# Performance work log

Measured on AMD Instinct MI355X. Metric: run time of the kernel, lower is better.

Reference implementation:

```python
import jax, jax.numpy as jnp
import numpy as np

N, M, D = 8192, 8192, 64

def setup_inputs() -> dict:
    key = jax.random.key(0)
    kx, ky = jax.random.split(key)
    x = jax.random.normal(kx, (N, D), dtype=jnp.float32)
    y = jax.random.normal(ky, (M, D), dtype=jnp.float32)
    return {"x": x, "y": y}

def reference(x, y):
    T = 1.0
    # Dmat = 2 - euclidean cdist(x, y), computed via the Gram trick.
    sq = (jnp.sum(x * x, axis=1)[:, None]
          + jnp.sum(y * y, axis=1)[None, :]
          - 2.0 * (x @ y.T))
    Dmat = 2.0 - jnp.sqrt(jnp.maximum(sq, 0.0))          # [N, M]
    logprob_rows = jax.nn.log_softmax(Dmat * T, axis=1)   # [N, M]
    logprob_cols = jax.nn.log_softmax(Dmat.T * T, axis=1) # [M, N]
    choice_rows = jnp.argmax(logprob_rows, axis=1)        # [N]
    choice_cols = jnp.argmax(logprob_cols, axis=1)        # [M]
    seq = jnp.arange(M, dtype=choice_cols.dtype)
    mutual = choice_rows[choice_cols] == seq              # [M] bool
    lp_rows = jnp.take_along_axis(logprob_rows, choice_rows[:, None], axis=1)[:, 0]  # [N]
    lp_cols = jnp.take_along_axis(logprob_cols, choice_cols[:, None], axis=1)[:, 0]  # [M]
    # Padded (jit-friendly) form of the boolean compaction: entries where
    # mutual is False are zeroed; mutual mask identifies valid matches.
    log_probs = jnp.where(mutual, lp_rows[choice_cols] + lp_cols, 0.0)  # [M]
    dmatches = jnp.stack([choice_cols, seq], axis=1)      # [M, 2]
    return (log_probs, dmatches, mutual)
```

## Files before the change

### kernel.cpp

```cpp
#include <hip/hip_runtime.h>
#include <stdint.h>

#define NROWS 8192
#define MCOLS 8192
#define DDIM  64
#define NBX   32
#define NBY   64

typedef _Float16 half8   __attribute__((ext_vector_type(8)));
typedef float    floatx4 __attribute__((ext_vector_type(4)));

__device__ __forceinline__ unsigned f2key(float f) {
  unsigned u = __float_as_uint(f);
  return (u & 0x80000000u) ? ~u : (u | 0x80000000u);
}
__device__ __forceinline__ float key2f(unsigned k) {
  unsigned u = (k & 0x80000000u) ? (k & 0x7fffffffu) : ~k;
  return __uint_as_float(u);
}

__global__ void convert_kernel(const float* __restrict__ x, const float* __restrict__ y,
                               _Float16* __restrict__ xh, _Float16* __restrict__ xl,
                               _Float16* __restrict__ yh, _Float16* __restrict__ yl,
                               float* __restrict__ xn, float* __restrict__ yn) {
  __shared__ float lnorm[32];
  const int gid = blockIdx.x * 256 + threadIdx.x;
  if (threadIdx.x < 32) lnorm[threadIdx.x] = 0.0f;
  __syncthreads();

  const float* src; _Float16 *dh, *dl; float* nout; int t, rowbase;
  if (gid < 65536) { src = x; dh = xh; dl = xl; nout = xn; t = gid;
                     rowbase = blockIdx.x * 32; }
  else             { src = y; dh = yh; dl = yl; nout = yn; t = gid - 65536;
                     rowbase = (blockIdx.x - 256) * 32; }

  const int lane = t & 63;
  const int c    = (t >> 6) & 1;
  const int p    = t >> 7;
  const int row  = p * 16 + (lane & 15);
  const int k0   = c * 32 + ((lane >> 4) << 3);
  const float* s = src + (size_t)row * DDIM + k0;

  float fb[8];
  *(floatx4*)(&fb[0]) = *(const floatx4*)(s);
  *(floatx4*)(&fb[4]) = *(const floatx4*)(s + 4);

  _Float16 hbuf[8], lbuf[8];
  float s8 = 0.0f;
  #pragma unroll
  for (int j = 0; j < 8; ++j) {
    float f = fb[j];
    _Float16 h = (_Float16)f;
    hbuf[j] = h;
    lbuf[j] = (_Float16)((f - (float)h) * 2048.0f);
    s8 = fmaf(f, f, s8);
  }
  size_t o = (size_t)t * 8;
  *(half8*)(dh + o) = *(half8*)hbuf;
  *(half8*)(dl + o) = *(half8*)lbuf;

  atomicAdd(&lnorm[((p & 1) << 4) | (t & 15)], s8);
  __syncthreads();
  if (threadIdx.x < 32) nout[rowbase + threadIdx.x] = lnorm[threadIdx.x];
}

#define MFMA16(A, B, C) __builtin_amdgcn_mfma_f32_16x16x32_f16((A), (B), (C), 0, 0, 0)

__global__ __launch_bounds__(256, 3) void mfma_tile_kernel(
    const _Float16* __restrict__ xh, const _Float16* __restrict__ xl,
    const _Float16* __restrict__ yh, const _Float16* __restrict__ yl,
    const float* __restrict__ xn, const float* __restrict__ yn,
    unsigned long long* __restrict__ row_part_key, float* __restrict__ row_part_sum,
    unsigned long long* __restrict__ col_part_key, float* __restrict__ col_part_sum)
{
  __shared__ unsigned long long lkey[256];
  __shared__ float              lsum[256];

  const int wave = threadIdx.x >> 6;
  const int lane = threadIdx.x & 63;
  const int l15  = lane & 15;
  const int g    = lane >> 4;
  const int ap0  = blockIdx.y * 8 + wave * 2;
  const int ro   = ap0 * 16 + g * 4;
  const int colbase = blockIdx.x * 256;

  lkey[threadIdx.x] = 0ull;
  lsum[threadIdx.x] = 0.0f;
  __syncthreads();

  const half8* xh8 = (const half8*)xh;
  const half8* xl8 = (const half8*)xl;
  const half8* yh8 = (const half8*)yh;
  const half8* yl8 = (const half8*)yl;
  const size_t a0 = (size_t)ap0 * 128 + lane;
  half8 Ah[2][2], Al[2][2];
  #pragma unroll
  for (int p = 0; p < 2; ++p) {
    Ah[p][0] = xh8[a0 + p * 128];      Ah[p][1] = xh8[a0 + p * 128 + 64];
    Al[p][0] = xl8[a0 + p * 128];      Al[p][1] = xl8[a0 + p * 128 + 64];
  }

  float xne[8], rsum[8], rmax[8]; int ridx[8];
  #pragma unroll
  for (int s = 0; s < 8; ++s) {
    xne[s]  = xn[ro + ((s >> 2) << 4) + (s & 3)];
    rsum[s] = 0.0f; rmax[s] = -3.4e38f; ridx[s] = 0;
  }

  const size_t bcol0 = (size_t)(blockIdx.x * 16) * 128 + lane;

  half8 b0h0, b0h1, b0l0, b0l1; float y0n;
  half8 b1h0, b1h1, b1l0, b1l1; float y1n;
  b0h0 = yh8[bcol0];        b0h1 = yh8[bcol0 + 64];
  b0l0 = yl8[bcol0];        b0l1 = yl8[bcol0 + 64];
  y0n  = yn[colbase + l15];
  b1h0 = yh8[bcol0 + 128];  b1h1 = yh8[bcol0 + 192];
  b1l0 = yl8[bcol0 + 128];  b1l1 = yl8[bcol0 + 192];
  y1n  = yn[colbase + 16 + l15];

#define MFMA_TILE(BH0, BH1, BL0, BL1, O1A, O2A, O1B, O2B)                      \
  {                                                                            \
    floatx4 c1_ = {}, c2_ = {};                                                \
    c1_ = MFMA16(Ah[0][0], BH0, c1_);                                          \
    c1_ = MFMA16(Ah[0][1], BH1, c1_);                                          \
    c2_ = MFMA16(Al[0][0], BH0, c2_);                                          \
    c2_ = MFMA16(Al[0][1], BH1, c2_);                                          \
    c2_ = MFMA16(Ah[0][0], BL0, c2_);                                          \
    c2_ = MFMA16(Ah[0][1], BL1, c2_);                                          \
    O1A = c1_; O2A = c2_;                                                      \
    floatx4 d1_ = {}, d2_ = {};                                                \
    d1_ = MFMA16(Ah[1][0], BH0, d1_);                                          \
    d1_ = MFMA16(Ah[1][1], BH1, d1_);                                          \
    d2_ = MFMA16(Al[1][0], BH0, d2_);                                          \
    d2_ = MFMA16(Al[1][1], BH1, d2_);                                          \
    d2_ = MFMA16(Ah[1][0], BL0, d2_);                                          \
    d2_ = MFMA16(Ah[1][1], BL1, d2_);                                          \
    O1B = d1_; O2B = d2_;                                                      \
  }

#define EPILOGUE(JT, C1A, C2A, C1B, C2B, YNC)                                  \
  {                                                                            \
    const int col_ = colbase + (JT) * 16 + l15;                                \
    float cmax_ = -3.4e38f; int cidx_ = 0;                                     \
    float epan0_, epan1_;                                                      \
    {                                                                          \
      float ee_[4];                                                            \
      _Pragma("unroll")                                                        \
      for (int r = 0; r < 4; ++r) {                                            \
        const int s_ = r;                                                      \
        float dot = fmaf(C2A[r], (1.0f / 2048.0f), C1A[r]);                    \
        float sq  = fmaxf(fmaf(-2.0f, dot, xne[s_] + (YNC)), 0.0f);            \
        float d   = 2.0f - __builtin_amdgcn_sqrtf(sq);                         \
        float e   = __expf(d);                                                 \
        rsum[s_] += e;                                                         \
        if (d > rmax[s_]) ridx[s_] = col_;       \
        rmax[s_] = fmaxf(rmax[s_], d);                                         \
        if (d > cmax_) cidx_ = s_;               \
        cmax_ = fmaxf(cmax_, d);                                               \
        ee_[r] = e;                                                            \
      }                                                                        \
      epan0_ = (ee_[0] + ee_[1]) + (ee_[2] + ee_[3]);                          \
    }                                                                          \
    {                                                                          \
      float ee_[4];                                                            \
      _Pragma("unroll")                                                        \
      for (int r = 0; r < 4; ++r) {                                            \
        const int s_ = 4 + r;                                                  \
        float dot = fmaf(C2B[r], (1.0f / 2048.0f), C1B[r]);                    \
        float sq  = fmaxf(fmaf(-2.0f, dot, xne[s_] + (YNC)), 0.0f);            \
        float d   = 2.0f - __builtin_amdgcn_sqrtf(sq);                         \
        float e   = __expf(d);                                                 \
        rsum[s_] += e;                                                         \
        if (d > rmax[s_]) ridx[s_] = col_;                                     \
        rmax[s_] = fmaxf(rmax[s_], d);                                         \
        if (d > cmax_) cidx_ = s_;                                             \
        cmax_ = fmaxf(cmax_, d);                                               \
        ee_[r] = e;                                                            \
      }                                                                        \
      epan1_ = (ee_[0] + ee_[1]) + (ee_[2] + ee_[3]);                          \
    }                                                                          \
    float csum_ = epan0_ + epan1_;                \
    int crow_ = ro + ((cidx_ >> 2) << 4) + (cidx_ & 3);                        \
    unsigned long long ckey_ =                                                 \
        ((unsigned long long)f2key(cmax_) << 32) |                             \
        (unsigned long long)(unsigned)(~(unsigned)crow_);                      \
    atomicMax(&lkey[(JT) * 16 + l15], ckey_);                  \
    atomicAdd(&lsum[(JT) * 16 + l15], csum_);                  \
  }

  floatx4 Pc1a, Pc2a, Pc1b, Pc2b;
  floatx4 Qc1a, Qc2a, Qc1b, Qc2b;

  MFMA_TILE(b0h0, b0h1, b0l0, b0l1, Pc1a, Pc2a, Pc1b, Pc2b);

  for (int jt = 0; jt < 14; jt += 2) {
    {
      float ycur = y0n;
      const size_t bn = bcol0 + (size_t)(jt + 2) * 128;
      b0h0 = yh8[bn];      b0h1 = yh8[bn + 64];
      b0l0 = yl8[bn];      b0l1 = yl8[bn + 64];
      y0n  = yn[colbase + (jt + 2) * 16 + l15];
      MFMA_TILE(b1h0, b1h1, b1l0, b1l1, Qc1a, Qc2a, Qc1b, Qc2b);
      EPILOGUE(jt, Pc1a, Pc2a, Pc1b, Pc2b, ycur);
    }
    {
      float ycur = y1n;
      const size_t bn = bcol0 + (size_t)(jt + 3) * 128;
      b1h0 = yh8[bn];      b1h1 = yh8[bn + 64];
      b1l0 = yl8[bn];      b1l1 = yl8[bn + 64];
      y1n  = yn[colbase + (jt + 3) * 16 + l15];
      MFMA_TILE(b0h0, b0h1, b0l0, b0l1, Pc1a, Pc2a, Pc1b, Pc2b);
      EPILOGUE(jt + 1, Qc1a, Qc2a, Qc1b, Qc2b, ycur);
    }
  }
  {
    MFMA_TILE(b1h0, b1h1, b1l0, b1l1, Qc1a, Qc2a, Qc1b, Qc2b);
    EPILOGUE(14, Pc1a, Pc2a, Pc1b, Pc2b, y0n);
  }
  EPILOGUE(15, Qc1a, Qc2a, Qc1b, Qc2b, y1n);

#undef MFMA_TILE
#undef EPILOGUE

  unsigned long long rkk[8];
  #pragma unroll
  for (int s = 0; s < 8; ++s)
    rkk[s] = ((unsigned long long)f2key(rmax[s]) << 32) |
             (unsigned long long)(unsigned)(~(unsigned)ridx[s]);
  #pragma unroll
  for (int off = 1; off < 16; off <<= 1) {
    #pragma unroll
    for (int s = 0; s < 8; ++s) {
      rsum[s] += __shfl_xor(rsum[s], off);
      unsigned long long o = __shfl_xor(rkk[s], off);
      if (o > rkk[s]) rkk[s] = o;
    }
  }
  if (l15 == 0) {
    #pragma unroll
    for (int s = 0; s < 8; ++s) {
      int row = ro + ((s >> 2) << 4) + (s & 3);
      row_part_key[(size_t)blockIdx.x * NROWS + row] = rkk[s];
      row_part_sum[(size_t)blockIdx.x * NROWS + row] = rsum[s];
    }
  }

  __syncthreads();
  {
    int col = colbase + threadIdx.x;
    col_part_key[(size_t)blockIdx.y * MCOLS + col] = lkey[threadIdx.x];
    col_part_sum[(size_t)blockIdx.y * MCOLS + col] = lsum[threadIdx.x];
  }
}

__global__ __launch_bounds__(256) void reduce_rows_kernel(
    const unsigned long long* __restrict__ rpk,
    const float* __restrict__ rps,
    unsigned long long* __restrict__ row_key,
    float* __restrict__ row_sum)
{
  const int t   = blockIdx.x * 256 + threadIdx.x;
  const int row = t >> 3;
  const int i   = t & 7;
  unsigned long long best = 0ull; float sum = 0.0f;
  #pragma unroll
  for (int k = 0; k < 4; ++k) {
    const int bx = i + k * 8;
    unsigned long long kk = rpk[(size_t)bx * NROWS + row];
    if (kk > best) best = kk;
    sum += rps[(size_t)bx * NROWS + row];
  }
  #pragma unroll
  for (int off = 1; off < 8; off <<= 1) {
    sum += __shfl_xor(sum, off);
    unsigned long long o = __shfl_xor(best, off);
    if (o > best) best = o;
  }
  if (i == 0) { row_key[row] = best; row_sum[row] = sum; }
}

__global__ __launch_bounds__(256) void finalize_kernel(
    const unsigned long long* __restrict__ row_key,
    const float* __restrict__ row_sum,
    const unsigned long long* __restrict__ cpk,
    const float* __restrict__ cps,
    float* __restrict__ out)
{
  const int t = blockIdx.x * 256 + threadIdx.x;
  const int j = t >> 3;
  const int i = t & 7;

  unsigned long long ck = 0ull; float csum = 0.0f;
  #pragma unroll
  for (int k = 0; k < 8; ++k) {
    const int by = i + k * 8;
    unsigned long long kk = cpk[(size_t)by * MCOLS + j];
    if (kk > ck) ck = kk;
    csum += cps[(size_t)by * MCOLS + j];
  }
  #pragma unroll
  for (int off = 1; off < 8; off <<= 1) {
    csum += __shfl_xor(csum, off);
    unsigned long long o = __shfl_xor(ck, off);
    if (o > ck) ck = o;
  }
  if (i != 0) return;

  int   ci   = (int)(~(unsigned)ck);
  float cmax = key2f((unsigned)(ck >> 32));
  float lp_col = cmax - logf(csum);

  unsigned long long rk = row_key[ci];
  int   rj   = (int)(~(unsigned)rk);
  float rmax = key2f((unsigned)(rk >> 32));
  float lp_row = rmax - logf(row_sum[ci]);

  int mut = (rj == j);
  out[j]                 = mut ? (lp_row + lp_col) : 0.0f;
  out[MCOLS + 2 * j + 0] = (float)ci;
  out[MCOLS + 2 * j + 1] = (float)j;
  out[3 * MCOLS + j]     = mut ? 1.0f : 0.0f;
}

extern "C" void kernel_launch(void* const* d_in, const int* in_sizes, int n_in,
                              void* d_out, int out_size, void* d_ws, size_t ws_size,
                              hipStream_t stream) {
  const float* x = (const float*)d_in[0];
  const float* y = (const float*)d_in[1];
  float* out = (float*)d_out;

  char* ws = (char*)d_ws;
  unsigned long long* row_key = (unsigned long long*)(ws);
  float* row_sum = (float*)(ws + 65536);
  float* xn      = (float*)(ws + 98304);
  float* yn      = (float*)(ws + 131072);
  unsigned long long* rpk = (unsigned long long*)(ws + 163840);
  float* rps     = (float*)(ws + 2260992);
  unsigned long long* cpk = (unsigned long long*)(ws + 3309568);
  float* cps     = (float*)(ws + 7503872);
  _Float16* xh = (_Float16*)(ws + 9601024);
  _Float16* xl = (_Float16*)(ws + 10649600);
  _Float16* yh = (_Float16*)(ws + 11698176);
  _Float16* yl = (_Float16*)(ws + 12746752);

  convert_kernel<<<512, 256, 0, stream>>>(x, y, xh, xl, yh, yl, xn, yn);
  dim3 grid(MCOLS / 256, NROWS / 128);
  mfma_tile_kernel<<<grid, 256, 0, stream>>>(xh, xl, yh, yl, xn, yn,
                                             rpk, rps, cpk, cps);
  reduce_rows_kernel<<<256, 256, 0, stream>>>(rpk, rps, row_key, row_sum);
  finalize_kernel<<<256, 256, 0, stream>>>(row_key, row_sum, cpk, cps, out);
}
```

Measured before the change: 123.5 us.

## Split row panels across eight waves and fuse row reduction into finalize

The main tile kernel now launches 512 threads per block, with each wave handling a single 16-row panel instead of two. This lowers per-wave register pressure and raises latency hiding, at the cost of loading the B fragments twice as often per block. The separate row-reduction kernel is removed. Finalize instead reduces the partial row keys and sums only for each column's chosen row, which saves a launch and a full pass over the row partials.

```diff
diff --git a/kernel.cpp b/kernel.cpp
--- a/kernel.cpp
+++ b/kernel.cpp
@@ -66,7 +66,7 @@
 
 #define MFMA16(A, B, C) __builtin_amdgcn_mfma_f32_16x16x32_f16((A), (B), (C), 0, 0, 0)
 
-__global__ __launch_bounds__(256, 3) void mfma_tile_kernel(
+__global__ __launch_bounds__(512, 2) void mfma_tile_kernel(
     const _Float16* __restrict__ xh, const _Float16* __restrict__ xl,
     const _Float16* __restrict__ yh, const _Float16* __restrict__ yl,
     const float* __restrict__ xn, const float* __restrict__ yn,
@@ -80,30 +80,25 @@
   const int lane = threadIdx.x & 63;
   const int l15  = lane & 15;
   const int g    = lane >> 4;
-  const int ap0  = blockIdx.y * 8 + wave * 2;
-  const int ro   = ap0 * 16 + g * 4;
+  const int ap   = blockIdx.y * 8 + wave;
+  const int ro   = ap * 16 + g * 4;
   const int colbase = blockIdx.x * 256;
 
-  lkey[threadIdx.x] = 0ull;
-  lsum[threadIdx.x] = 0.0f;
+  if (threadIdx.x < 256) { lkey[threadIdx.x] = 0ull; lsum[threadIdx.x] = 0.0f; }
   __syncthreads();
 
   const half8* xh8 = (const half8*)xh;
   const half8* xl8 = (const half8*)xl;
   const half8* yh8 = (const half8*)yh;
   const half8* yl8 = (const half8*)yl;
-  const size_t a0 = (size_t)ap0 * 128 + lane;
-  half8 Ah[2][2], Al[2][2];
-  #pragma unroll
-  for (int p = 0; p < 2; ++p) {
-    Ah[p][0] = xh8[a0 + p * 128];      Ah[p][1] = xh8[a0 + p * 128 + 64];
-    Al[p][0] = xl8[a0 + p * 128];      Al[p][1] = xl8[a0 + p * 128 + 64];
-  }
-
-  float xne[8], rsum[8], rmax[8]; int ridx[8];
-  #pragma unroll
-  for (int s = 0; s < 8; ++s) {
-    xne[s]  = xn[ro + ((s >> 2) << 4) + (s & 3)];
+  const size_t a0 = (size_t)ap * 128 + lane;
+  half8 Ah0 = xh8[a0], Ah1 = xh8[a0 + 64];
+  half8 Al0 = xl8[a0], Al1 = xl8[a0 + 64];
+
+  float xne[4], rsum[4], rmax[4]; int ridx[4];
+  #pragma unroll
+  for (int s = 0; s < 4; ++s) {
+    xne[s]  = xn[ro + s];
     rsum[s] = 0.0f; rmax[s] = -3.4e38f; ridx[s] = 0;
   }
 
@@ -118,69 +113,38 @@
   b1l0 = yl8[bcol0 + 128];  b1l1 = yl8[bcol0 + 192];
   y1n  = yn[colbase + 16 + l15];
 
-#define MFMA_TILE(BH0, BH1, BL0, BL1, O1A, O2A, O1B, O2B)                      \
+#define MFMA_TILE(BH0, BH1, BL0, BL1, O1, O2)                                  \
   {                                                                            \
     floatx4 c1_ = {}, c2_ = {};                                                \
-    c1_ = MFMA16(Ah[0][0], BH0, c1_);                                          \
-    c1_ = MFMA16(Ah[0][1], BH1, c1_);                                          \
-    c2_ = MFMA16(Al[0][0], BH0, c2_);                                          \
-    c2_ = MFMA16(Al[0][1], BH1, c2_);                                          \
-    c2_ = MFMA16(Ah[0][0], BL0, c2_);                                          \
-    c2_ = MFMA16(Ah[0][1], BL1, c2_);                                          \
-    O1A = c1_; O2A = c2_;                                                      \
-    floatx4 d1_ = {}, d2_ = {};                                                \
-    d1_ = MFMA16(Ah[1][0], BH0, d1_);                                          \
-    d1_ = MFMA16(Ah[1][1], BH1, d1_);                                          \
-    d2_ = MFMA16(Al[1][0], BH0, d2_);                                          \
-    d2_ = MFMA16(Al[1][1], BH1, d2_);                                          \
-    d2_ = MFMA16(Ah[1][0], BL0, d2_);                                          \
-    d2_ = MFMA16(Ah[1][1], BL1, d2_);                                          \
-    O1B = d1_; O2B = d2_;                                                      \
-  }
-
-#define EPILOGUE(JT, C1A, C2A, C1B, C2B, YNC)                                  \
+    c1_ = MFMA16(Ah0, BH0, c1_);                                               \
+    c1_ = MFMA16(Ah1, BH1, c1_);                                               \
+    c2_ = MFMA16(Al0, BH0, c2_);                                               \
+    c2_ = MFMA16(Al1, BH1, c2_);                                               \
+    c2_ = MFMA16(Ah0, BL0, c2_);                                               \
+    c2_ = MFMA16(Ah1, BL1, c2_);                                               \
+    O1 = c1_; O2 = c2_;                                                        \
+  }
+
+#define EPILOGUE(JT, C1, C2, YNC)                                              \
   {                                                                            \
     const int col_ = colbase + (JT) * 16 + l15;                                \
     float cmax_ = -3.4e38f; int cidx_ = 0;                                     \
-    float epan0_, epan1_;                                                      \
-    {                                                                          \
-      float ee_[4];                                                            \
-      _Pragma("unroll")                                                        \
-      for (int r = 0; r < 4; ++r) {                                            \
-        const int s_ = r;                                                      \
-        float dot = fmaf(C2A[r], (1.0f / 2048.0f), C1A[r]);                    \
-        float sq  = fmaxf(fmaf(-2.0f, dot, xne[s_] + (YNC)), 0.0f);            \
-        float d   = 2.0f - __builtin_amdgcn_sqrtf(sq);                         \
-        float e   = __expf(d);                                                 \
-        rsum[s_] += e;                                                         \
-        if (d > rmax[s_]) ridx[s_] = col_;       \
-        rmax[s_] = fmaxf(rmax[s_], d);                                         \
-        if (d > cmax_) cidx_ = s_;               \
-        cmax_ = fmaxf(cmax_, d);                                               \
-        ee_[r] = e;                                                            \
-      }                                                                        \
-      epan0_ = (ee_[0] + ee_[1]) + (ee_[2] + ee_[3]);                          \
+    float ee_[4];                                                              \
+    _Pragma("unroll")                                                          \
+    for (int r = 0; r < 4; ++r) {                                              \
+      float dot = fmaf(C2[r], (1.0f / 2048.0f), C1[r]);                        \
+      float sq  = fmaxf(fmaf(-2.0f, dot, xne[r] + (YNC)), 0.0f);               \
+      float d   = 2.0f - __builtin_amdgcn_sqrtf(sq);                           \
+      float e   = __expf(d);                                                   \
+      rsum[r] += e;                                                            \
+      if (d > rmax[r]) ridx[r] = col_;           \
+      rmax[r] = fmaxf(rmax[r], d);                                             \
+      if (d > cmax_) cidx_ = r;                  \
+      cmax_ = fmaxf(cmax_, d);                                                 \
+      ee_[r] = e;                                                              \
     }                                                                          \
-    {                                                                          \
-      float ee_[4];                                                            \
-      _Pragma("unroll")                                                        \
-      for (int r = 0; r < 4; ++r) {                                            \
-        const int s_ = 4 + r;                                                  \
-        float dot = fmaf(C2B[r], (1.0f / 2048.0f), C1B[r]);                    \
-        float sq  = fmaxf(fmaf(-2.0f, dot, xne[s_] + (YNC)), 0.0f);            \
-        float d   = 2.0f - __builtin_amdgcn_sqrtf(sq);                         \
-        float e   = __expf(d);                                                 \
-        rsum[s_] += e;                                                         \
-        if (d > rmax[s_]) ridx[s_] = col_;                                     \
-        rmax[s_] = fmaxf(rmax[s_], d);                                         \
-        if (d > cmax_) cidx_ = s_;                                             \
-        cmax_ = fmaxf(cmax_, d);                                               \
-        ee_[r] = e;                                                            \
-      }                                                                        \
-      epan1_ = (ee_[0] + ee_[1]) + (ee_[2] + ee_[3]);                          \
-    }                                                                          \
-    float csum_ = epan0_ + epan1_;                \
-    int crow_ = ro + ((cidx_ >> 2) << 4) + (cidx_ & 3);                        \
+    float csum_ = (ee_[0] + ee_[1]) + (ee_[2] + ee_[3]);                       \
+    int crow_ = ro + cidx_;                                                    \
     unsigned long long ckey_ =                                                 \
         ((unsigned long long)f2key(cmax_) << 32) |                             \
         (unsigned long long)(unsigned)(~(unsigned)crow_);                      \
@@ -188,10 +152,9 @@
     atomicAdd(&lsum[(JT) * 16 + l15], csum_);                  \
   }
 
-  floatx4 Pc1a, Pc2a, Pc1b, Pc2b;
-  floatx4 Qc1a, Qc2a, Qc1b, Qc2b;
-
-  MFMA_TILE(b0h0, b0h1, b0l0, b0l1, Pc1a, Pc2a, Pc1b, Pc2b);
+  floatx4 Pc1, Pc2, Qc1, Qc2;
+
+  MFMA_TILE(b0h0, b0h1, b0l0, b0l1, Pc1, Pc2);
 
   for (int jt = 0; jt < 14; jt += 2) {
     {
@@ -200,8 +163,8 @@
       b0h0 = yh8[bn];      b0h1 = yh8[bn + 64];
       b0l0 = yl8[bn];      b0l1 = yl8[bn + 64];
       y0n  = yn[colbase + (jt + 2) * 16 + l15];
-      MFMA_TILE(b1h0, b1h1, b1l0, b1l1, Qc1a, Qc2a, Qc1b, Qc2b);
-      EPILOGUE(jt, Pc1a, Pc2a, Pc1b, Pc2b, ycur);
+      MFMA_TILE(b1h0, b1h1, b1l0, b1l1, Qc1, Qc2);
+      EPILOGUE(jt, Pc1, Pc2, ycur);
     }
     {
       float ycur = y1n;
@@ -209,28 +172,28 @@
       b1h0 = yh8[bn];      b1h1 = yh8[bn + 64];
       b1l0 = yl8[bn];      b1l1 = yl8[bn + 64];
       y1n  = yn[colbase + (jt + 3) * 16 + l15];
-      MFMA_TILE(b0h0, b0h1, b0l0, b0l1, Pc1a, Pc2a, Pc1b, Pc2b);
-      EPILOGUE(jt + 1, Qc1a, Qc2a, Qc1b, Qc2b, ycur);
+      MFMA_TILE(b0h0, b0h1, b0l0, b0l1, Pc1, Pc2);
+      EPILOGUE(jt + 1, Qc1, Qc2, ycur);
     }
   }
   {
-    MFMA_TILE(b1h0, b1h1, b1l0, b1l1, Qc1a, Qc2a, Qc1b, Qc2b);
-    EPILOGUE(14, Pc1a, Pc2a, Pc1b, Pc2b, y0n);
-  }
-  EPILOGUE(15, Qc1a, Qc2a, Qc1b, Qc2b, y1n);
+    MFMA_TILE(b1h0, b1h1, b1l0, b1l1, Qc1, Qc2);
+    EPILOGUE(14, Pc1, Pc2, y0n);
+  }
+  EPILOGUE(15, Qc1, Qc2, y1n);
 
 #undef MFMA_TILE
 #undef EPILOGUE
 
-  unsigned long long rkk[8];
-  #pragma unroll
-  for (int s = 0; s < 8; ++s)
+  unsigned long long rkk[4];
+  #pragma unroll
+  for (int s = 0; s < 4; ++s)
     rkk[s] = ((unsigned long long)f2key(rmax[s]) << 32) |
              (unsigned long long)(unsigned)(~(unsigned)ridx[s]);
   #pragma unroll
   for (int off = 1; off < 16; off <<= 1) {
     #pragma unroll
-    for (int s = 0; s < 8; ++s) {
+    for (int s = 0; s < 4; ++s) {
       rsum[s] += __shfl_xor(rsum[s], off);
       unsigned long long o = __shfl_xor(rkk[s], off);
       if (o > rkk[s]) rkk[s] = o;
@@ -238,50 +201,24 @@
   }
   if (l15 == 0) {
     #pragma unroll
-    for (int s = 0; s < 8; ++s) {
-      int row = ro + ((s >> 2) << 4) + (s & 3);
+    for (int s = 0; s < 4; ++s) {
+      int row = ro + s;
       row_part_key[(size_t)blockIdx.x * NROWS + row] = rkk[s];
       row_part_sum[(size_t)blockIdx.x * NROWS + row] = rsum[s];
     }
   }
 
   __syncthreads();
-  {
+  if (threadIdx.x < 256) {
     int col = colbase + threadIdx.x;
     col_part_key[(size_t)blockIdx.y * MCOLS + col] = lkey[threadIdx.x];
     col_part_sum[(size_t)blockIdx.y * MCOLS + col] = lsum[threadIdx.x];
   }
 }
 
-__global__ __launch_bounds__(256) void reduce_rows_kernel(
+__global__ __launch_bounds__(256) void finalize_kernel(
     const unsigned long long* __restrict__ rpk,
     const float* __restrict__ rps,
-    unsigned long long* __restrict__ row_key,
-    float* __restrict__ row_sum)
-{
-  const int t   = blockIdx.x * 256 + threadIdx.x;
-  const int row = t >> 3;
-  const int i   = t & 7;
-  unsigned long long best = 0ull; float sum = 0.0f;
-  #pragma unroll
-  for (int k = 0; k < 4; ++k) {
-    const int bx = i + k * 8;
-    unsigned long long kk = rpk[(size_t)bx * NROWS + row];
-    if (kk > best) best = kk;
-    sum += rps[(size_t)bx * NROWS + row];
-  }
-  #pragma unroll
-  for (int off = 1; off < 8; off <<= 1) {
-    sum += __shfl_xor(sum, off);
-    unsigned long long o = __shfl_xor(best, off);
-    if (o > best) best = o;
-  }
-  if (i == 0) { row_key[row] = best; row_sum[row] = sum; }
-}
-
-__global__ __launch_bounds__(256) void finalize_kernel(
-    const unsigned long long* __restrict__ row_key,
-    const float* __restrict__ row_sum,
     const unsigned long long* __restrict__ cpk,
     const float* __restrict__ cps,
     float* __restrict__ out)
@@ -304,16 +241,31 @@
     unsigned long long o = __shfl_xor(ck, off);
     if (o > ck) ck = o;
   }
+
+  const int ci = (int)(~(unsigned)ck);
+
+  unsigned long long rk = 0ull; float rsum = 0.0f;
+  #pragma unroll
+  for (int k = 0; k < 4; ++k) {
+    const int bx = i + k * 8;
+    unsigned long long kk = rpk[(size_t)bx * NROWS + ci];
+    if (kk > rk) rk = kk;
+    rsum += rps[(size_t)bx * NROWS + ci];
+  }
+  #pragma unroll
+  for (int off = 1; off < 8; off <<= 1) {
+    rsum += __shfl_xor(rsum, off);
+    unsigned long long o = __shfl_xor(rk, off);
+    if (o > rk) rk = o;
+  }
   if (i != 0) return;
 
-  int   ci   = (int)(~(unsigned)ck);
   float cmax = key2f((unsigned)(ck >> 32));
   float lp_col = cmax - logf(csum);
 
-  unsigned long long rk = row_key[ci];
   int   rj   = (int)(~(unsigned)rk);
   float rmax = key2f((unsigned)(rk >> 32));
-  float lp_row = rmax - logf(row_sum[ci]);
+  float lp_row = rmax - logf(rsum);
 
   int mut = (rj == j);
   out[j]                 = mut ? (lp_row + lp_col) : 0.0f;
@@ -330,23 +282,20 @@
   float* out = (float*)d_out;
 
   char* ws = (char*)d_ws;
-  unsigned long long* row_key = (unsigned long long*)(ws);
-  float* row_sum = (float*)(ws + 65536);
-  float* xn      = (float*)(ws + 98304);
-  float* yn      = (float*)(ws + 131072);
-  unsigned long long* rpk = (unsigned long long*)(ws + 163840);
-  float* rps     = (float*)(ws + 2260992);
-  unsigned long long* cpk = (unsigned long long*)(ws + 3309568);
-  float* cps     = (float*)(ws + 7503872);
-  _Float16* xh = (_Float16*)(ws + 9601024);
-  _Float16* xl = (_Float16*)(ws + 10649600);
-  _Float16* yh = (_Float16*)(ws + 11698176);
-  _Float16* yl = (_Float16*)(ws + 12746752);
+  float* xn      = (float*)(ws);
+  float* yn      = (float*)(ws + 32768);
+  unsigned long long* rpk = (unsigned long long*)(ws + 65536);
+  float* rps     = (float*)(ws + 2162688);
+  unsigned long long* cpk = (unsigned long long*)(ws + 3211264);
+  float* cps     = (float*)(ws + 7405568);
+  _Float16* xh = (_Float16*)(ws + 9502720);
+  _Float16* xl = (_Float16*)(ws + 10551296);
+  _Float16* yh = (_Float16*)(ws + 11599872);
+  _Float16* yl = (_Float16*)(ws + 12648448);
 
   convert_kernel<<<512, 256, 0, stream>>>(x, y, xh, xl, yh, yl, xn, yn);
   dim3 grid(MCOLS / 256, NROWS / 128);
-  mfma_tile_kernel<<<grid, 256, 0, stream>>>(xh, xl, yh, yl, xn, yn,
+  mfma_tile_kernel<<<grid, 512, 0, stream>>>(xh, xl, yh, yl, xn, yn,
                                              rpk, rps, cpk, cps);
-  reduce_rows_kernel<<<256, 256, 0, stream>>>(rpk, rps, row_key, row_sum);
-  finalize_kernel<<<256, 256, 0, stream>>>(row_key, row_sum, cpk, cps, out);
-}
+  finalize_kernel<<<256, 256, 0, stream>>>(rpk, rps, cpk, cps, out);
+}
```

New measurement: 164.2 us. +33.0%, slower.
